# Kernel optimization log

Measured on AMD Instinct MI355X. Metric: run time of the kernel, lower is better.

## Reference

```python
import jax, jax.numpy as jnp
import numpy as np

D_MODEL, N_HEAD, D_FF = 768, 12, 3072
HEAD_DIM = D_MODEL // N_HEAD
EPS = 1e-5


def _layernorm(x, g, b):
    mu = jnp.mean(x, axis=-1, keepdims=True)
    var = jnp.mean((x - mu) ** 2, axis=-1, keepdims=True)
    return (x - mu) * jax.lax.rsqrt(var + EPS) * g + b


def setup_inputs() -> dict:
    key = jax.random.key(0)
    ks = jax.random.split(key, 14)
    s = 1.0 / np.sqrt(D_MODEL)
    sf = 1.0 / np.sqrt(D_FF)
    inp = {
        "x": jax.random.normal(ks[0], (2, 2048, D_MODEL), dtype=jnp.float32),
        "Wq": jax.random.normal(ks[1], (D_MODEL, D_MODEL), dtype=jnp.float32) * s,
        "bq": jnp.zeros((D_MODEL,), jnp.float32),
        "Wk": jax.random.normal(ks[2], (D_MODEL, D_MODEL), dtype=jnp.float32) * s,
        "bk": jnp.zeros((D_MODEL,), jnp.float32),
        "Wv": jax.random.normal(ks[3], (D_MODEL, D_MODEL), dtype=jnp.float32) * s,
        "bv": jnp.zeros((D_MODEL,), jnp.float32),
        "Wo": jax.random.normal(ks[4], (D_MODEL, D_MODEL), dtype=jnp.float32) * s,
        "bo": jnp.zeros((D_MODEL,), jnp.float32),
        "W1": jax.random.normal(ks[5], (D_MODEL, D_FF), dtype=jnp.float32) * s,
        "b1": jnp.zeros((D_FF,), jnp.float32),
        "W2": jax.random.normal(ks[6], (D_FF, D_MODEL), dtype=jnp.float32) * sf,
        "b2": jnp.zeros((D_MODEL,), jnp.float32),
        "ln1_g": jnp.ones((D_MODEL,), jnp.float32),
        "ln1_b": jnp.zeros((D_MODEL,), jnp.float32),
        "ln2_g": jnp.ones((D_MODEL,), jnp.float32),
        "ln2_b": jnp.zeros((D_MODEL,), jnp.float32),
    }
    return inp


def reference(x, Wq, bq, Wk, bk, Wv, bv, Wo, bo, W1, b1, W2, b2,
              ln1_g, ln1_b, ln2_g, ln2_b):
    B, S, D = x.shape
    # projections -> [B, H, S, hd]
    def proj(W, b):
        return (x @ W + b).reshape(B, S, N_HEAD, HEAD_DIM).transpose(0, 2, 1, 3)
    q, k, v = proj(Wq, bq), proj(Wk, bk), proj(Wv, bv)
    scores = jnp.einsum("bhqd,bhkd->bhqk", q, k) / jnp.sqrt(
        jnp.asarray(HEAD_DIM, jnp.float32))
    attn = jax.nn.softmax(scores, axis=-1)
    ctx = jnp.einsum("bhqk,bhkd->bhqd", attn, v)
    ctx = ctx.transpose(0, 2, 1, 3).reshape(B, S, D)
    attn_out = ctx @ Wo + bo
    h = _layernorm(x + attn_out, ln1_g, ln1_b)
    ffn = jax.nn.gelu(h @ W1 + b1, approximate=False) @ W2 + b2
    return _layernorm(h + ffn, ln2_g, ln2_b)
```

## Files before the change

### kernel.cpp

```cpp
#include <hip/hip_runtime.h>
#include <hip/hip_bf16.h>
#include <cstdint>
#include <cstddef>

typedef unsigned short u16;
typedef __bf16 bf16x8 __attribute__((ext_vector_type(8)));
typedef float f32x4 __attribute__((ext_vector_type(4)));

#define MFMA_BF16(a, b, c) __builtin_amdgcn_mfma_f32_16x16x32_bf16((a), (b), (c), 0, 0, 0)

#define GLDS16(g, l)                                                        \
  __builtin_amdgcn_global_load_lds(                                         \
      (__attribute__((address_space(1))) void*)(void*)(g),                  \
      (__attribute__((address_space(3))) void*)(void*)(l), 16, 0, 0)

#define QSCALE 0.18033688011112042f
#define PSTRIDE ((size_t)4096 * 768)

__device__ __forceinline__ u16 f2bf(float x) {
  union { float f; unsigned u; } c; c.f = x;
  unsigned u = c.u;
  unsigned r = (u + 0x7fffu + ((u >> 16) & 1u)) >> 16;
  return (u16)r;
}


__global__ __launch_bounds__(256) void transpose_bf16_k(
    const float* __restrict__ in, u16* __restrict__ out, int K, int N) {
  __shared__ float tile[32][33];
  const int tx = threadIdx.x & 31, ty = threadIdx.x >> 5;
  const int bx = blockIdx.x * 32;
  const int by = blockIdx.y * 32;
#pragma unroll
  for (int j = 0; j < 32; j += 8)
    tile[ty + j][tx] = in[(size_t)(by + ty + j) * N + bx + tx];
  __syncthreads();
#pragma unroll
  for (int j = 0; j < 32; j += 8)
    out[(size_t)(bx + ty + j) * K + by + tx] = f2bf(tile[tx][ty + j]);
}

__global__ __launch_bounds__(256) void cvt_bf16_k(
    const float* __restrict__ in, u16* __restrict__ out, int n) {
  int i = (blockIdx.x * 256 + threadIdx.x) * 4;
  if (i + 3 < n) {
    const float4 v = *(const float4*)(in + i);
    ushort4 o;
    o.x = f2bf(v.x); o.y = f2bf(v.y); o.z = f2bf(v.z); o.w = f2bf(v.w);
    *(ushort4*)(out + i) = o;
  }
}

__global__ __launch_bounds__(256) void concat3_k(
    const float* __restrict__ a, const float* __restrict__ b,
    const float* __restrict__ c, float* __restrict__ out) {
  int i = blockIdx.x * 256 + threadIdx.x;
  if (i < 768) out[i] = a[i];
  else if (i < 1536) out[i] = b[i - 768];
  else if (i < 2304) out[i] = c[i - 1536];
}

template <int EPI>
__global__ __launch_bounds__(256) void gemm_bt(
    const u16* __restrict__ A, const u16* __restrict__ BT,
    const float* __restrict__ bias, int M, int N, int K, int kchunk,
    float* __restrict__ outf, u16* __restrict__ outb,
    u16* __restrict__ qo, u16* __restrict__ ko, u16* __restrict__ vto) {
  __shared__ __align__(16) u16 lsA[128 * 64];
  __shared__ __align__(16) u16 lsB[128 * 64];
  const int tid = threadIdx.x;
  const int w = tid >> 6, lane = tid & 63;
  const int wm = w & 1, wn = w >> 1;
  const int lrow = lane & 15, quad = lane >> 4;
  const int m0 = blockIdx.y * 128, n0 = blockIdx.x * 128;
  const int kbeg = blockIdx.z * kchunk, kend = kbeg + kchunk;

  f32x4 acc[4][4];
#pragma unroll
  for (int i = 0; i < 4; ++i)
#pragma unroll
    for (int j = 0; j < 4; ++j) acc[i][j] = (f32x4){0.f, 0.f, 0.f, 0.f};

  const int off = tid * 16;
  const int srow = off >> 7;
  const int schunk = (off >> 4) & 7;
  const int sxc = schunk ^ (srow & 7);
  const int scol = sxc * 8;

  const int rsw = lrow & 7;

  for (int k0 = kbeg; k0 < kend; k0 += 64) {
    const u16* ga = A + (size_t)(m0 + srow) * K + k0 + scol;
    const u16* gb = BT + (size_t)(n0 + srow) * K + k0 + scol;
#pragma unroll
    for (int c = 0; c < 4; ++c) {
      GLDS16(ga + (size_t)(c * 32) * K, (char*)lsA + c * 4096 + off);
      GLDS16(gb + (size_t)(c * 32) * K, (char*)lsB + c * 4096 + off);
    }
    __syncthreads();
#pragma unroll
    for (int ks = 0; ks < 2; ++ks) {
      const int slot = ((ks * 4 + quad) ^ rsw) * 8;
      bf16x8 af[4], bfr[4];
#pragma unroll
      for (int ms = 0; ms < 4; ++ms)
        af[ms] = *(const bf16x8*)&lsA[(wm * 64 + ms * 16 + lrow) * 64 + slot];
#pragma unroll
      for (int ns = 0; ns < 4; ++ns)
        bfr[ns] = *(const bf16x8*)&lsB[(wn * 64 + ns * 16 + lrow) * 64 + slot];
#pragma unroll
      for (int ms = 0; ms < 4; ++ms)
#pragma unroll
        for (int ns = 0; ns < 4; ++ns)
          acc[ms][ns] = MFMA_BF16(af[ms], bfr[ns], acc[ms][ns]);
    }
    __syncthreads();
  }

  float* const pf = (EPI == 3) ? outf + (size_t)blockIdx.z * M * N : outf;
#pragma unroll
  for (int ms = 0; ms < 4; ++ms) {
    const int rbase = m0 + wm * 64 + ms * 16 + quad * 4;
#pragma unroll
    for (int ns = 0; ns < 4; ++ns) {
      const int col = n0 + wn * 64 + ns * 16 + lrow;
      if constexpr (EPI == 3) {
#pragma unroll
        for (int r = 0; r < 4; ++r)
          pf[(size_t)(rbase + r) * N + col] = acc[ms][ns][r];
      } else if constexpr (EPI == 2) {
        const float bcol = bias[col];
#pragma unroll
        for (int r = 0; r < 4; ++r) {
          float v = acc[ms][ns][r] + bcol;
          float g = 0.5f * v * (1.0f + erff(v * 0.7071067811865476f));
          outb[(size_t)(rbase + r) * N + col] = f2bf(g);
        }
      } else {
        const float bcol = bias[col];
        const int which = col / 768;
        const int rem = col - which * 768;
        const int hh = rem >> 6, dd = rem & 63;
        const int bI = rbase >> 11, sI = rbase & 2047;
        const size_t bh = (size_t)bI * 12 + hh;
        if (which == 0) {
#pragma unroll
          for (int r = 0; r < 4; ++r)
            qo[(bh * 2048 + sI + r) * 64 + dd] = f2bf((acc[ms][ns][r] + bcol) * QSCALE);
        } else if (which == 1) {
#pragma unroll
          for (int r = 0; r < 4; ++r)
            ko[(bh * 2048 + sI + r) * 64 + dd] = f2bf(acc[ms][ns][r] + bcol);
        } else {
          ushort4 pk;
          pk.x = f2bf(acc[ms][ns][0] + bcol);
          pk.y = f2bf(acc[ms][ns][1] + bcol);
          pk.z = f2bf(acc[ms][ns][2] + bcol);
          pk.w = f2bf(acc[ms][ns][3] + bcol);
          *(ushort4*)(vto + (bh * 64 + dd) * 2048 + sI) = pk;
        }
      }
    }
  }
}

__global__ __launch_bounds__(256) void attn_kernel(
    const u16* __restrict__ q, const u16* __restrict__ k,
    const u16* __restrict__ vT, u16* __restrict__ opart,
    float* __restrict__ lpart) {
  __shared__ __align__(16) u16 lsK[2 * 64 * 64];
  __shared__ __align__(16) u16 lsV[2 * 64 * 64];
  __shared__ __align__(16) u16 lsP[4][16 * 64];
  const int tid = threadIdx.x;
  const int w = tid >> 6, lane = tid & 63;
  const int lrow = lane & 15, quad = lane >> 4;
  const int bh = blockIdx.y;
  const int b = bh / 12, h = bh - b * 12;
  const int q0 = blockIdx.x * 64;
  const int z = blockIdx.z;
  const int kvbeg = z * 1024;

  const u16* qbase = q + (size_t)bh * 2048 * 64;
  const u16* kbase = k + (size_t)bh * 2048 * 64;
  const u16* vbase = vT + (size_t)bh * 64 * 2048;

  const int qrow = q0 + w * 16 + lrow;
  const bf16x8 qf0 = *(const bf16x8*)(qbase + (size_t)qrow * 64 + quad * 8);
  const bf16x8 qf1 = *(const bf16x8*)(qbase + (size_t)qrow * 64 + 32 + quad * 8);

  float lsum[4] = {0.f, 0.f, 0.f, 0.f};
  f32x4 oacc[4];
#pragma unroll
  for (int d = 0; d < 4; ++d) oacc[d] = (f32x4){0.f, 0.f, 0.f, 0.f};

  const int off = tid * 16;
  const int srow = off >> 7;
  const int schunk = (off >> 4) & 7;
  const int sxc = schunk ^ (srow & 7);
  const int ksrc = srow * 64 + sxc * 8;
  const int vsrc0 = srow * 2048 + sxc * 8;

  const int c0 = quad ^ (lrow & 7);
  const int rd0 = c0 * 8, rd1 = (c0 ^ 4) * 8;

  u16* const lsPw = &lsP[w][0];
  const int jhi_base = lrow >> 3, jlo = lrow & 7;

  auto stage = [&](int kt, int buf) {
    char* dk = (char*)(lsK + buf * 4096);
    char* dv = (char*)(lsV + buf * 4096);
    GLDS16(kbase + (size_t)kt * 64 + ksrc, dk + off);
    GLDS16(kbase + (size_t)(kt + 32) * 64 + ksrc, dk + 4096 + off);
    GLDS16(vbase + vsrc0 + kt, dv + off);
    GLDS16(vbase + vsrc0 + kt + 32 * 2048, dv + 4096 + off);
  };

  stage(kvbeg, 0);
  for (int t = 0; t < 16; ++t) {
    __syncthreads();
    if (t < 15) stage(kvbeg + (t + 1) * 64, (t + 1) & 1);
    const u16* Kb = lsK + (t & 1) * 4096;
    const u16* Vb = lsV + (t & 1) * 4096;

    f32x4 sc[4];
#pragma unroll
    for (int ns = 0; ns < 4; ++ns) {
      sc[ns] = (f32x4){0.f, 0.f, 0.f, 0.f};
      const u16* kr = Kb + (ns * 16 + lrow) * 64;
      bf16x8 kf0 = *(const bf16x8*)(kr + rd0);
      bf16x8 kf1 = *(const bf16x8*)(kr + rd1);
      sc[ns] = MFMA_BF16(qf0, kf0, sc[ns]);
      sc[ns] = MFMA_BF16(qf1, kf1, sc[ns]);
    }

#pragma unroll
    for (int ns = 0; ns < 4; ++ns) {
      const int jhi = ns * 2 + jhi_base;
#pragma unroll
      for (int r = 0; r < 4; ++r) {
        float p = __builtin_amdgcn_exp2f(sc[ns][r]);
        lsum[r] += p;
        union { float f; unsigned u; } cv; cv.f = p;
        const int m = quad * 4 + r;
        lsPw[m * 64 + ((jhi ^ (m & 7)) * 8) + jlo] = (u16)(cv.u >> 16);
      }
    }

    const u16* pr = lsPw + lrow * 64;
    const bf16x8 pf0 = *(const bf16x8*)(pr + rd0);
    const bf16x8 pf1 = *(const bf16x8*)(pr + rd1);
#pragma unroll
    for (int d = 0; d < 4; ++d) {
      const u16* vr = Vb + (d * 16 + lrow) * 64;
      bf16x8 vf0 = *(const bf16x8*)(vr + rd0);
      bf16x8 vf1 = *(const bf16x8*)(vr + rd1);
      oacc[d] = MFMA_BF16(pf0, vf0, oacc[d]);
      oacc[d] = MFMA_BF16(pf1, vf1, oacc[d]);
    }
  }

#pragma unroll
  for (int r = 0; r < 4; ++r) {
#pragma unroll
    for (int mm = 1; mm <= 8; mm <<= 1) lsum[r] += __shfl_xor(lsum[r], mm);
  }

  const int srow_out = q0 + w * 16 + quad * 4;
  u16* const op = opart + (size_t)z * PSTRIDE;
#pragma unroll
  for (int d = 0; d < 4; ++d)
#pragma unroll
    for (int r = 0; r < 4; ++r)
      op[(size_t)(b * 2048 + srow_out + r) * 768 + h * 64 + d * 16 + lrow] =
          f2bf(oacc[d][r]);
  if (lrow == 0) {
#pragma unroll
    for (int r = 0; r < 4; ++r)
      lpart[(size_t)(z * 24 + bh) * 2048 + srow_out + r] = lsum[r];
  }
}

__global__ __launch_bounds__(256) void attn_combine_k(
    const u16* __restrict__ op, const float* __restrict__ lp,
    u16* __restrict__ ctx) {
  const int row = blockIdx.x;
  const int b = row >> 11, s = row & 2047;
  const int tid = threadIdx.x;
#pragma unroll
  for (int j = 0; j < 3; ++j) {
    const int c = tid + j * 256;
    const int h = c >> 6;
    const size_t li = (size_t)(b * 12 + h) * 2048 + s;
    const float l = lp[li] + lp[(size_t)24 * 2048 + li];
    union { unsigned u; float f; } a0, a1;
    a0.u = (unsigned)op[(size_t)row * 768 + c] << 16;
    a1.u = (unsigned)op[PSTRIDE + (size_t)row * 768 + c] << 16;
    ctx[(size_t)row * 768 + c] = f2bf((a0.f + a1.f) / l);
  }
}

__global__ __launch_bounds__(256) void ln_kernel(
    const float* __restrict__ parts, int nparts, const float* __restrict__ bias,
    const float* __restrict__ res, const float* __restrict__ g,
    const float* __restrict__ bb, float* __restrict__ outf, u16* __restrict__ outb) {
  const int row = blockIdx.x;
  const int tid = threadIdx.x;
  const float* pr = res + (size_t)row * 768;
  float v[3], s = 0.f, s2 = 0.f;
#pragma unroll
  for (int j = 0; j < 3; ++j) {
    const int c = tid + j * 256;
    float t = bias[c] + pr[c];
    for (int p = 0; p < nparts; ++p)
      t += parts[p * PSTRIDE + (size_t)row * 768 + c];
    v[j] = t; s += t; s2 += t * t;
  }
#pragma unroll
  for (int m = 32; m > 0; m >>= 1) {
    s += __shfl_xor(s, m);
    s2 += __shfl_xor(s2, m);
  }
  __shared__ float red[8];
  const int w = tid >> 6, lane = tid & 63;
  if (lane == 0) { red[w] = s; red[4 + w] = s2; }
  __syncthreads();
  s = red[0] + red[1] + red[2] + red[3];
  s2 = red[4] + red[5] + red[6] + red[7];
  const float mu = s * (1.f / 768.f);
  const float var = s2 * (1.f / 768.f) - mu * mu;
  const float rstd = rsqrtf(var + 1e-5f);
#pragma unroll
  for (int j = 0; j < 3; ++j) {
    const int c = tid + j * 256;
    const float y = (v[j] - mu) * rstd * g[c] + bb[c];
    if (outf) outf[(size_t)row * 768 + c] = y;
    if (outb) outb[(size_t)row * 768 + c] = f2bf(y);
  }
}

extern "C" void kernel_launch(void* const* d_in, const int* in_sizes, int n_in,
                              void* d_out, int out_size, void* d_ws, size_t ws_size,
                              hipStream_t stream) {
  const float* x    = (const float*)d_in[0];
  const float* Wq   = (const float*)d_in[1];
  const float* bq   = (const float*)d_in[2];
  const float* Wk   = (const float*)d_in[3];
  const float* bk   = (const float*)d_in[4];
  const float* Wv   = (const float*)d_in[5];
  const float* bv   = (const float*)d_in[6];
  const float* Wo   = (const float*)d_in[7];
  const float* bo   = (const float*)d_in[8];
  const float* W1   = (const float*)d_in[9];
  const float* b1   = (const float*)d_in[10];
  const float* W2   = (const float*)d_in[11];
  const float* b2   = (const float*)d_in[12];
  const float* ln1g = (const float*)d_in[13];
  const float* ln1b = (const float*)d_in[14];
  const float* ln2g = (const float*)d_in[15];
  const float* ln2b = (const float*)d_in[16];

  char* ws = (char*)d_ws;
  size_t off = 0;
  auto alloc = [&](size_t bytes) {
    void* p = ws + off;
    off += (bytes + 255) & ~(size_t)255;
    return p;
  };
  u16*  WqkvT = (u16*)alloc(2304ull * 768 * 2);
  u16*  WoT   = (u16*)alloc(768ull * 768 * 2);
  u16*  W1T   = (u16*)alloc(3072ull * 768 * 2);
  u16*  W2T   = (u16*)alloc(768ull * 3072 * 2);
  float* bqkv = (float*)alloc(2304 * 4);
  char* bigbase = (char*)alloc(0);
  u16*  xb    = (u16*)alloc(4096ull * 768 * 2);
  u16*  qb    = (u16*)alloc(24ull * 2048 * 64 * 2);
  u16*  kb    = (u16*)alloc(24ull * 2048 * 64 * 2);
  u16*  vtb   = (u16*)alloc(24ull * 64 * 2048 * 2);
  u16*  ctx   = (u16*)alloc(4096ull * 768 * 2);
  float* attno = (float*)alloc(2ull * PSTRIDE * 4);
  float* f2b   = (float*)bigbase;
  u16*   opart = (u16*)attno;
  float* lpart = (float*)((char*)attno + 2 * PSTRIDE * 2);
  float* hbuf  = (float*)alloc(4096ull * 768 * 4);
  u16*  hb    = (u16*)alloc(4096ull * 768 * 2);
  u16*  f1    = (u16*)alloc(4096ull * 3072 * 2);

  transpose_bf16_k<<<dim3(24, 24), 256, 0, stream>>>(Wq, WqkvT, 768, 768);
  transpose_bf16_k<<<dim3(24, 24), 256, 0, stream>>>(Wk, WqkvT + 768 * 768, 768, 768);
  transpose_bf16_k<<<dim3(24, 24), 256, 0, stream>>>(Wv, WqkvT + 2 * 768 * 768, 768, 768);
  transpose_bf16_k<<<dim3(24, 24), 256, 0, stream>>>(Wo, WoT, 768, 768);
  transpose_bf16_k<<<dim3(96, 24), 256, 0, stream>>>(W1, W1T, 768, 3072);
  transpose_bf16_k<<<dim3(24, 96), 256, 0, stream>>>(W2, W2T, 3072, 768);
  concat3_k<<<9, 256, 0, stream>>>(bq, bk, bv, bqkv);
  cvt_bf16_k<<<3072, 256, 0, stream>>>(x, xb, 4096 * 768);

  gemm_bt<0><<<dim3(18, 32, 1), 256, 0, stream>>>(xb, WqkvT, bqkv, 4096, 2304, 768, 768,
                                                  nullptr, nullptr, qb, kb, vtb);
  attn_kernel<<<dim3(32, 24, 2), 256, 0, stream>>>(qb, kb, vtb, opart, lpart);
  attn_combine_k<<<4096, 256, 0, stream>>>(opart, lpart, ctx);
  gemm_bt<3><<<dim3(6, 32, 2), 256, 0, stream>>>(ctx, WoT, nullptr, 4096, 768, 768, 384,
                                                 attno, nullptr, nullptr, nullptr, nullptr);
  ln_kernel<<<4096, 256, 0, stream>>>(attno, 2, bo, x, ln1g, ln1b, hbuf, hb);
  gemm_bt<2><<<dim3(24, 32, 1), 256, 0, stream>>>(hb, W1T, b1, 4096, 3072, 768, 768,
                                                  nullptr, f1, nullptr, nullptr, nullptr);
  gemm_bt<3><<<dim3(6, 32, 4), 256, 0, stream>>>(f1, W2T, nullptr, 4096, 768, 3072, 768,
                                                 f2b, nullptr, nullptr, nullptr, nullptr);
  ln_kernel<<<4096, 256, 0, stream>>>(f2b, 4, b2, hbuf, ln2g, ln2b, (float*)d_out, nullptr);
}
```

Before: 326.6 us.

## Process two query tiles per wave in attention and vectorize combine kernel

Each attention wave now handles 32 query rows instead of 16, so one set of K/V LDS fragment loads feeds two MFMA row-tiles. This halves the grid and roughly halves the K/V staging traffic per query row. The attention combine kernel is rewritten so each thread handles four contiguous elements with vector loads and a reciprocal multiply. The cost is higher register and LDS use per block and fewer blocks to fill the GPU.

```diff
diff --git a/kernel.cpp b/kernel.cpp
--- a/kernel.cpp
+++ b/kernel.cpp
@@ -170,13 +170,13 @@
     float* __restrict__ lpart) {
   __shared__ __align__(16) u16 lsK[2 * 64 * 64];
   __shared__ __align__(16) u16 lsV[2 * 64 * 64];
-  __shared__ __align__(16) u16 lsP[4][16 * 64];
+  __shared__ __align__(16) u16 lsP[4][32 * 64];
   const int tid = threadIdx.x;
   const int w = tid >> 6, lane = tid & 63;
   const int lrow = lane & 15, quad = lane >> 4;
   const int bh = blockIdx.y;
   const int b = bh / 12, h = bh - b * 12;
-  const int q0 = blockIdx.x * 64;
+  const int q0 = blockIdx.x * 128;
   const int z = blockIdx.z;
   const int kvbeg = z * 1024;
 
@@ -184,14 +184,20 @@
   const u16* kbase = k + (size_t)bh * 2048 * 64;
   const u16* vbase = vT + (size_t)bh * 64 * 2048;
 
-  const int qrow = q0 + w * 16 + lrow;
-  const bf16x8 qf0 = *(const bf16x8*)(qbase + (size_t)qrow * 64 + quad * 8);
-  const bf16x8 qf1 = *(const bf16x8*)(qbase + (size_t)qrow * 64 + 32 + quad * 8);
-
-  float lsum[4] = {0.f, 0.f, 0.f, 0.f};
-  f32x4 oacc[4];
-#pragma unroll
-  for (int d = 0; d < 4; ++d) oacc[d] = (f32x4){0.f, 0.f, 0.f, 0.f};
+  bf16x8 qf[2][2];
+#pragma unroll
+  for (int m = 0; m < 2; ++m) {
+    const int qrow = q0 + w * 32 + m * 16 + lrow;
+    qf[m][0] = *(const bf16x8*)(qbase + (size_t)qrow * 64 + quad * 8);
+    qf[m][1] = *(const bf16x8*)(qbase + (size_t)qrow * 64 + 32 + quad * 8);
+  }
+
+  float lsum[2][4] = {{0.f, 0.f, 0.f, 0.f}, {0.f, 0.f, 0.f, 0.f}};
+  f32x4 oacc[2][4];
+#pragma unroll
+  for (int m = 0; m < 2; ++m)
+#pragma unroll
+    for (int d = 0; d < 4; ++d) oacc[m][d] = (f32x4){0.f, 0.f, 0.f, 0.f};
 
   const int off = tid * 16;
   const int srow = off >> 7;
@@ -222,81 +228,99 @@
     const u16* Kb = lsK + (t & 1) * 4096;
     const u16* Vb = lsV + (t & 1) * 4096;
 
-    f32x4 sc[4];
+    f32x4 sc[2][4];
 #pragma unroll
     for (int ns = 0; ns < 4; ++ns) {
-      sc[ns] = (f32x4){0.f, 0.f, 0.f, 0.f};
       const u16* kr = Kb + (ns * 16 + lrow) * 64;
       bf16x8 kf0 = *(const bf16x8*)(kr + rd0);
       bf16x8 kf1 = *(const bf16x8*)(kr + rd1);
-      sc[ns] = MFMA_BF16(qf0, kf0, sc[ns]);
-      sc[ns] = MFMA_BF16(qf1, kf1, sc[ns]);
-    }
-
-#pragma unroll
-    for (int ns = 0; ns < 4; ++ns) {
-      const int jhi = ns * 2 + jhi_base;
-#pragma unroll
-      for (int r = 0; r < 4; ++r) {
-        float p = __builtin_amdgcn_exp2f(sc[ns][r]);
-        lsum[r] += p;
-        union { float f; unsigned u; } cv; cv.f = p;
-        const int m = quad * 4 + r;
-        lsPw[m * 64 + ((jhi ^ (m & 7)) * 8) + jlo] = (u16)(cv.u >> 16);
+#pragma unroll
+      for (int m = 0; m < 2; ++m) {
+        sc[m][ns] = (f32x4){0.f, 0.f, 0.f, 0.f};
+        sc[m][ns] = MFMA_BF16(qf[m][0], kf0, sc[m][ns]);
+        sc[m][ns] = MFMA_BF16(qf[m][1], kf1, sc[m][ns]);
       }
     }
 
-    const u16* pr = lsPw + lrow * 64;
-    const bf16x8 pf0 = *(const bf16x8*)(pr + rd0);
-    const bf16x8 pf1 = *(const bf16x8*)(pr + rd1);
+#pragma unroll
+    for (int m = 0; m < 2; ++m)
+#pragma unroll
+      for (int ns = 0; ns < 4; ++ns) {
+        const int jhi = ns * 2 + jhi_base;
+#pragma unroll
+        for (int r = 0; r < 4; ++r) {
+          float p = __builtin_amdgcn_exp2f(sc[m][ns][r]);
+          lsum[m][r] += p;
+          union { float f; unsigned u; } cv; cv.f = p;
+          const int row7 = (quad * 4 + r) & 7;
+          lsPw[(m * 16 + quad * 4 + r) * 64 + ((jhi ^ row7) * 8) + jlo] =
+              (u16)(cv.u >> 16);
+        }
+      }
+
 #pragma unroll
     for (int d = 0; d < 4; ++d) {
       const u16* vr = Vb + (d * 16 + lrow) * 64;
       bf16x8 vf0 = *(const bf16x8*)(vr + rd0);
       bf16x8 vf1 = *(const bf16x8*)(vr + rd1);
-      oacc[d] = MFMA_BF16(pf0, vf0, oacc[d]);
-      oacc[d] = MFMA_BF16(pf1, vf1, oacc[d]);
-    }
-  }
-
-#pragma unroll
-  for (int r = 0; r < 4; ++r) {
-#pragma unroll
-    for (int mm = 1; mm <= 8; mm <<= 1) lsum[r] += __shfl_xor(lsum[r], mm);
-  }
-
-  const int srow_out = q0 + w * 16 + quad * 4;
+#pragma unroll
+      for (int m = 0; m < 2; ++m) {
+        const u16* pr = lsPw + (m * 16 + lrow) * 64;
+        bf16x8 pf0 = *(const bf16x8*)(pr + rd0);
+        bf16x8 pf1 = *(const bf16x8*)(pr + rd1);
+        oacc[m][d] = MFMA_BF16(pf0, vf0, oacc[m][d]);
+        oacc[m][d] = MFMA_BF16(pf1, vf1, oacc[m][d]);
+      }
+    }
+  }
+
+#pragma unroll
+  for (int m = 0; m < 2; ++m)
+#pragma unroll
+    for (int r = 0; r < 4; ++r) {
+#pragma unroll
+      for (int mm = 1; mm <= 8; mm <<= 1)
+        lsum[m][r] += __shfl_xor(lsum[m][r], mm);
+    }
+
   u16* const op = opart + (size_t)z * PSTRIDE;
 #pragma unroll
-  for (int d = 0; d < 4; ++d)
-#pragma unroll
-    for (int r = 0; r < 4; ++r)
-      op[(size_t)(b * 2048 + srow_out + r) * 768 + h * 64 + d * 16 + lrow] =
-          f2bf(oacc[d][r]);
-  if (lrow == 0) {
-#pragma unroll
-    for (int r = 0; r < 4; ++r)
-      lpart[(size_t)(z * 24 + bh) * 2048 + srow_out + r] = lsum[r];
+  for (int m = 0; m < 2; ++m) {
+    const int srow_out = q0 + w * 32 + m * 16 + quad * 4;
+#pragma unroll
+    for (int d = 0; d < 4; ++d)
+#pragma unroll
+      for (int r = 0; r < 4; ++r)
+        op[(size_t)(b * 2048 + srow_out + r) * 768 + h * 64 + d * 16 + lrow] =
+            f2bf(oacc[m][d][r]);
+    if (lrow == 0) {
+#pragma unroll
+      for (int r = 0; r < 4; ++r)
+        lpart[(size_t)(z * 24 + bh) * 2048 + srow_out + r] = lsum[m][r];
+    }
   }
 }
 
 __global__ __launch_bounds__(256) void attn_combine_k(
     const u16* __restrict__ op, const float* __restrict__ lp,
     u16* __restrict__ ctx) {
-  const int row = blockIdx.x;
+  const unsigned idx = (blockIdx.x * 256u + threadIdx.x) * 4u;
+  const unsigned row = idx / 768u;
+  const unsigned c = idx - row * 768u;
   const int b = row >> 11, s = row & 2047;
-  const int tid = threadIdx.x;
-#pragma unroll
-  for (int j = 0; j < 3; ++j) {
-    const int c = tid + j * 256;
-    const int h = c >> 6;
-    const size_t li = (size_t)(b * 12 + h) * 2048 + s;
-    const float l = lp[li] + lp[(size_t)24 * 2048 + li];
-    union { unsigned u; float f; } a0, a1;
-    a0.u = (unsigned)op[(size_t)row * 768 + c] << 16;
-    a1.u = (unsigned)op[PSTRIDE + (size_t)row * 768 + c] << 16;
-    ctx[(size_t)row * 768 + c] = f2bf((a0.f + a1.f) / l);
-  }
+  const int h = c >> 6;
+  const size_t li = (size_t)(b * 12 + h) * 2048 + s;
+  const float rinv = 1.f / (lp[li] + lp[(size_t)24 * 2048 + li]);
+  ushort4 o0 = *(const ushort4*)(op + idx);
+  ushort4 o1 = *(const ushort4*)(op + PSTRIDE + idx);
+  ushort4 out;
+  union { unsigned u; float f; } a, bb2;
+#define CMB(fld) \
+  a.u = (unsigned)o0.fld << 16; bb2.u = (unsigned)o1.fld << 16; \
+  out.fld = f2bf((a.f + bb2.f) * rinv);
+  CMB(x) CMB(y) CMB(z) CMB(w)
+#undef CMB
+  *(ushort4*)(ctx + idx) = out;
 }
 
 __global__ __launch_bounds__(256) void ln_kernel(
@@ -396,8 +420,8 @@
 
   gemm_bt<0><<<dim3(18, 32, 1), 256, 0, stream>>>(xb, WqkvT, bqkv, 4096, 2304, 768, 768,
                                                   nullptr, nullptr, qb, kb, vtb);
-  attn_kernel<<<dim3(32, 24, 2), 256, 0, stream>>>(qb, kb, vtb, opart, lpart);
-  attn_combine_k<<<4096, 256, 0, stream>>>(opart, lpart, ctx);
+  attn_kernel<<<dim3(16, 24, 2), 256, 0, stream>>>(qb, kb, vtb, opart, lpart);
+  attn_combine_k<<<3072, 256, 0, stream>>>(opart, lpart, ctx);
   gemm_bt<3><<<dim3(6, 32, 2), 256, 0, stream>>>(ctx, WoT, nullptr, 4096, 768, 768, 384,
                                                  attno, nullptr, nullptr, nullptr, nullptr);
   ln_kernel<<<4096, 256, 0, stream>>>(attno, 2, bo, x, ln1g, ln1b, hbuf, hb);
```

New measurement: 317.7 us. 2.7% less time.
